# Kernel optimization log

Hardware: AMD Instinct MI355X
Metric: run time of the kernel (lower is better)

Reference implementation:

```python
import jax, jax.numpy as jnp
import numpy as np

N = 50000; F = 128; H = 128; E = 800000; G = 512; C = 1000; CE = 64; L = 128
EPS = 1e-5

def gcn_conv(x, src, dst, W, b, num_nodes):
    # PyG GCNConv: add self loops, sym-normalize, aggregate at dst
    loop = jnp.arange(num_nodes)
    s = jnp.concatenate([src, loop])
    d = jnp.concatenate([dst, loop])
    deg = jax.ops.segment_sum(jnp.ones_like(d, dtype=x.dtype), d, num_segments=num_nodes)
    dinv = jnp.where(deg > 0, jax.lax.rsqrt(deg), 0.0)
    norm = dinv[s] * dinv[d]                      # [E+N]
    h = x @ W                                     # [N,H]
    msg = h[s] * norm[:, None]                    # gather + scale
    return jax.ops.segment_sum(msg, d, num_segments=num_nodes) + b

def layer_norm(x, w, b):
    mu = jnp.mean(x, axis=-1, keepdims=True)
    var = jnp.var(x, axis=-1, keepdims=True)
    return (x - mu) * jax.lax.rsqrt(var + EPS) * w + b

def setup_inputs() -> dict:
    key = jax.random.key(0)
    ks = jax.random.split(key, 16)
    x = jax.random.normal(ks[0], (N, F), dtype=jnp.float32)
    edge_index = jax.random.randint(ks[1], (2, E), 0, N)
    batch = jnp.sort(jax.random.randint(ks[2], (N,), 0, G))
    cell_lines = jax.random.randint(ks[3], (G,), 0, C)
    def kai(k, shape):
        fan_in = shape[0]
        bound = np.sqrt(6.0 / fan_in)
        return jax.random.uniform(k, shape, jnp.float32, -bound, bound)
    return {
        'x': x, 'edge_index': edge_index, 'batch': batch, 'cell_lines': cell_lines,
        'W1': kai(ks[4], (F, H)), 'b1': jnp.zeros((H,), jnp.float32),
        'W2': kai(ks[5], (H, H)), 'b2': jnp.zeros((H,), jnp.float32),
        'emb': jax.random.normal(ks[6], (C, CE), dtype=jnp.float32),
        'Wc': kai(ks[7], (H + CE, H)), 'bc': jnp.zeros((H,), jnp.float32),
        'lnc_w': jnp.ones((H,), jnp.float32), 'lnc_b': jnp.zeros((H,), jnp.float32),
        'Wf1': kai(ks[8], (H, H)), 'bf1': jnp.zeros((H,), jnp.float32),
        'ln1_w': jnp.ones((H,), jnp.float32), 'ln1_b': jnp.zeros((H,), jnp.float32),
        'Wf2': kai(ks[9], (H, L)), 'bf2': jnp.zeros((L,), jnp.float32),
    }

def reference(x, edge_index, batch, cell_lines, W1, b1, W2, b2, emb, Wc, bc,
              lnc_w, lnc_b, Wf1, bf1, ln1_w, ln1_b, Wf2, bf2):
    src, dst = edge_index[0], edge_index[1]
    h = jax.nn.relu(gcn_conv(x, src, dst, W1, b1, N))
    h = jax.nn.relu(gcn_conv(h, src, dst, W2, b2, N))
    g = jax.ops.segment_sum(h, batch, num_segments=G)          # global_add_pool [G,H]
    ce = emb[cell_lines]                                       # [G,CE]
    comb = jnp.concatenate([g, ce], axis=1)
    comb = jax.nn.relu(layer_norm(comb @ Wc + bc, lnc_w, lnc_b))
    out = jax.nn.relu(comb @ Wf1 + bf1)                        # dropout = identity (eval)
    out = layer_norm(out, ln1_w, ln1_b)
    return out @ Wf2 + bf2
```

## Files before the change

### kernel.cpp

```cpp
#include <hip/hip_runtime.h>

#define N_NODES 50000
#define NFEAT 128
#define NEDGE 800000
#define NGRAPH 512
#define NCE 64
#define EPS 1e-5f
#define NBUCK 196
#define EPB 4096
#define BCAP 6144

typedef short s8v __attribute__((ext_vector_type(8)));
typedef float f4v __attribute__((ext_vector_type(4)));

static __device__ __forceinline__ unsigned short f2bf(float f) {
    unsigned int u = __float_as_uint(f);
    unsigned int r = u + 0x7fffu + ((u >> 16) & 1u);
    return (unsigned short)(r >> 16);
}
static __device__ __forceinline__ float bf_lo(unsigned int packed) {
    return __uint_as_float(packed << 16);
}
static __device__ __forceinline__ float bf_hi(unsigned int packed) {
    return __uint_as_float(packed & 0xffff0000u);
}
static __device__ __forceinline__ float bf_us(unsigned short us) {
    return __uint_as_float(((unsigned int)us) << 16);
}

__global__ __launch_bounds__(256) void wcast_kernel(
    const float* __restrict__ W1, const float* __restrict__ W2,
    unsigned short* __restrict__ WT1, unsigned short* __restrict__ WT2,
    int* __restrict__ bucketCursor)
{
    if (blockIdx.x == 0 && blockIdx.y == 0 && threadIdx.x < NBUCK)
        bucketCursor[threadIdx.x] = 0;
    const float* W = blockIdx.y ? W2 : W1;
    unsigned short* WT = blockIdx.y ? WT2 : WT1;
    int idx = blockIdx.x * 256 + threadIdx.x;
    int k = idx >> 7, n = idx & 127;
    WT[n * 128 + k] = f2bf(W[idx]);
}

__global__ __launch_bounds__(256) void bucket_scatter_kernel(
    const int* __restrict__ ei, int* __restrict__ bucketCursor,
    unsigned int* __restrict__ recbuf, int E)
{
    __shared__ int hist[NBUCK];
    __shared__ int lbase[NBUCK];
    __shared__ int gbase[NBUCK];
    __shared__ int cur[NBUCK];
    __shared__ int scanbuf[256];
    __shared__ unsigned int staging[EPB];
    int tid = threadIdx.x;
    if (tid < NBUCK) { hist[tid] = 0; cur[tid] = 0; }
    __syncthreads();

    unsigned int rec[EPB / 256];
    int e0 = blockIdx.x * EPB + tid;
#pragma unroll
    for (int i = 0; i < EPB / 256; ++i) {
        int e = e0 + i * 256;
        if (e < E) {
            unsigned int sv = (unsigned)ei[e];
            unsigned int dv = (unsigned)ei[E + e];
            rec[i] = sv | (dv << 16);
            atomicAdd(&hist[dv >> 8], 1);
        } else {
            rec[i] = 0xffffffffu;
        }
    }
    __syncthreads();
    int v = (tid < NBUCK) ? hist[tid] : 0;
    scanbuf[tid] = v; __syncthreads();
    for (int off = 1; off < 256; off <<= 1) {
        int t = (tid >= off) ? scanbuf[tid - off] : 0;
        __syncthreads();
        scanbuf[tid] += t;
        __syncthreads();
    }
    if (tid < NBUCK) lbase[tid] = scanbuf[tid] - v;
    int total = scanbuf[255];
    if (tid < NBUCK) gbase[tid] = (v > 0) ? atomicAdd(&bucketCursor[tid], v) : 0;
    __syncthreads();
#pragma unroll
    for (int i = 0; i < EPB / 256; ++i) {
        if (rec[i] != 0xffffffffu) {
            int b = rec[i] >> 24;
            int loc = atomicAdd(&cur[b], 1);
            staging[lbase[b] + loc] = rec[i];
        }
    }
    __syncthreads();
    for (int s = tid; s < total; s += 256) {
        unsigned int r = staging[s];
        int b = r >> 24;
        int pos = gbase[b] + (s - lbase[b]);
        if (pos < BCAP) recbuf[(size_t)b * BCAP + pos] = r;
    }
}

__global__ __launch_bounds__(256) void bucket_csr_kernel(
    const unsigned int* __restrict__ recbuf, const int* __restrict__ bucketCursor,
    int* __restrict__ rowbeg, unsigned short* __restrict__ deg,
    float* __restrict__ dinv, unsigned short* __restrict__ colidx)
{
    __shared__ int cnt[256];
    __shared__ int cur[256];
    __shared__ int scanbuf[256];
    __shared__ unsigned short stage[BCAP];
    int b = blockIdx.x, tid = threadIdx.x;
    int base = b * BCAP;
    int len = bucketCursor[b]; if (len > BCAP) len = BCAP;
    cnt[tid] = 0;
    __syncthreads();
    for (int s = tid; s < len; s += 256) {
        unsigned int r = recbuf[base + s];
        atomicAdd(&cnt[(r >> 16) & 255], 1);
    }
    __syncthreads();
    int v = cnt[tid];
    scanbuf[tid] = v; __syncthreads();
    for (int off = 1; off < 256; off <<= 1) {
        int t = (tid >= off) ? scanbuf[tid - off] : 0;
        __syncthreads();
        scanbuf[tid] += t;
        __syncthreads();
    }
    int excl = scanbuf[tid] - v;
    int node = b * 256 + tid;
    if (node < N_NODES) {
        rowbeg[node] = base + excl;
        deg[node] = (unsigned short)v;
        dinv[node] = rsqrtf((float)v + 1.0f);
    }
    cur[tid] = excl;
    __syncthreads();
    for (int s = tid; s < len; s += 256) {
        unsigned int r = recbuf[base + s];
        int pos = atomicAdd(&cur[(r >> 16) & 255], 1);
        stage[pos] = (unsigned short)(r & 0xffffu);
    }
    __syncthreads();
    for (int s = tid; s < len; s += 256) colidx[base + s] = stage[s];
}

template<bool FP32IN>
__global__ __launch_bounds__(256) void gemm_mfma_kernel(
    const void* __restrict__ Ain, const unsigned short* __restrict__ WTg,
    const float* __restrict__ dinv, unsigned short* __restrict__ HS, int nrows)
{
    __shared__ unsigned short as[128 * 128];
    __shared__ unsigned short wt[128 * 128];
    const int tid = threadIdx.x;
    const int row0 = blockIdx.x * 128;

    {
        const uint4* src = reinterpret_cast<const uint4*>(WTg);
        uint4* dst = reinterpret_cast<uint4*>(wt);
#pragma unroll
        for (int i = 0; i < 8; ++i) dst[tid + i * 256] = src[tid + i * 256];
    }
    if (FP32IN) {
        const float* X = (const float*)Ain;
#pragma unroll
        for (int i = 0; i < 16; ++i) {
            int f = tid + i * 256;
            int r = f >> 5, c4 = f & 31;
            int rr = row0 + r; if (rr >= nrows) rr = nrows - 1;
            float4 v = *reinterpret_cast<const float4*>(&X[rr * 128 + c4 * 4]);
            ushort4 o;
            o.x = f2bf(v.x); o.y = f2bf(v.y); o.z = f2bf(v.z); o.w = f2bf(v.w);
            *reinterpret_cast<ushort4*>(&as[r * 128 + c4 * 4]) = o;
        }
    } else {
        const unsigned short* X = (const unsigned short*)Ain;
#pragma unroll
        for (int i = 0; i < 8; ++i) {
            int f = tid + i * 256;
            int r = f >> 4, c8 = f & 15;
            int rr = row0 + r; if (rr >= nrows) rr = nrows - 1;
            *reinterpret_cast<uint4*>(&as[r * 128 + c8 * 8]) =
                *reinterpret_cast<const uint4*>(&X[rr * 128 + c8 * 8]);
        }
    }
    __syncthreads();

    const int w = tid >> 6;
    const int lane = tid & 63;
    const int quad = lane >> 4;
    const int col0 = lane & 15;

    s8v afr[2][4];
#pragma unroll
    for (int rt = 0; rt < 2; ++rt)
#pragma unroll
        for (int kt = 0; kt < 4; ++kt)
            afr[rt][kt] = *reinterpret_cast<const s8v*>(
                &as[(w * 32 + rt * 16 + col0) * 128 + kt * 32 + quad * 8]);

    f4v acc[2][8];
#pragma unroll
    for (int rt = 0; rt < 2; ++rt)
#pragma unroll
        for (int nt = 0; nt < 8; ++nt)
            acc[rt][nt] = (f4v){0.f, 0.f, 0.f, 0.f};

#pragma unroll
    for (int nt = 0; nt < 8; ++nt) {
        s8v bfr[4];
#pragma unroll
        for (int kt = 0; kt < 4; ++kt)
            bfr[kt] = *reinterpret_cast<const s8v*>(
                &wt[(nt * 16 + col0) * 128 + kt * 32 + quad * 8]);
#pragma unroll
        for (int rt = 0; rt < 2; ++rt)
#pragma unroll
            for (int kt = 0; kt < 4; ++kt)
                acc[rt][nt] = __builtin_amdgcn_mfma_f32_16x16x32_bf16(
                    afr[rt][kt], bfr[kt], acc[rt][nt], 0, 0, 0);
    }

    float dv[2][4];
#pragma unroll
    for (int rt = 0; rt < 2; ++rt)
#pragma unroll
        for (int reg = 0; reg < 4; ++reg) {
            int r = row0 + w * 32 + rt * 16 + quad * 4 + reg;
            dv[rt][reg] = (r < nrows) ? dinv[r] : 0.f;
        }

#pragma unroll
    for (int rt = 0; rt < 2; ++rt)
#pragma unroll
        for (int nt = 0; nt < 8; ++nt)
#pragma unroll
            for (int reg = 0; reg < 4; ++reg) {
                int rl = w * 32 + rt * 16 + quad * 4 + reg;
                as[rl * 128 + nt * 16 + col0] = f2bf(acc[rt][nt][reg] * dv[rt][reg]);
            }
    __syncthreads();
#pragma unroll
    for (int i = 0; i < 8; ++i) {
        int f = tid + i * 256;
        int r = f >> 4, c8 = f & 15;
        if (row0 + r < nrows)
            *reinterpret_cast<uint4*>(&HS[(size_t)(row0 + r) * 128 + c8 * 8]) =
                *reinterpret_cast<const uint4*>(&as[r * 128 + c8 * 8]);
    }
}

__global__ __launch_bounds__(256) void aggregate_kernel(
    const uint2* __restrict__ H2,
    const int* __restrict__ rowbeg, const unsigned short* __restrict__ deg,
    const unsigned short* __restrict__ colidx,
    const float* __restrict__ dinv, const float* __restrict__ bias,
    uint2* __restrict__ OUT, int n)
{
    int wid = (blockIdx.x * blockDim.x + threadIdx.x) >> 6;
    int lane = threadIdx.x & 63;
    if (wid >= n) return;
    const int half = lane >> 5;
    const int sub = lane & 31;
    int beg = rowbeg[wid];
    int cnt = (int)deg[wid] + 1;
    float s0 = 0.f, s1 = 0.f, s2 = 0.f, s3 = 0.f;
    float r0 = 0.f, r1 = 0.f, r2 = 0.f, r3 = 0.f;
    for (int base = 0; base < cnt; base += 64) {
        int m = cnt - base; if (m > 64) m = 64;
        int p = base + lane;
        int idx = 0;
        if (lane < m) idx = (p == 0) ? wid : (int)colidx[beg + p - 1];
        int j = 0;
        for (; j + 16 <= m; j += 16) {
            uint2 t[8];
#pragma unroll
            for (int q = 0; q < 8; ++q) {
                int u = __shfl(idx, j + q * 2 + half);
                t[q] = H2[(size_t)u * 32 + sub];
            }
#pragma unroll
            for (int q = 0; q < 8; q += 2) {
                s0 += bf_lo(t[q].x); s1 += bf_hi(t[q].x);
                s2 += bf_lo(t[q].y); s3 += bf_hi(t[q].y);
                r0 += bf_lo(t[q + 1].x); r1 += bf_hi(t[q + 1].x);
                r2 += bf_lo(t[q + 1].y); r3 += bf_hi(t[q + 1].y);
            }
        }
        for (; j + 4 <= m; j += 4) {
            int ua = __shfl(idx, j + half);
            int ub = __shfl(idx, j + 2 + half);
            uint2 ta = H2[(size_t)ua * 32 + sub];
            uint2 tb = H2[(size_t)ub * 32 + sub];
            s0 += bf_lo(ta.x); s1 += bf_hi(ta.x);
            s2 += bf_lo(ta.y); s3 += bf_hi(ta.y);
            r0 += bf_lo(tb.x); r1 += bf_hi(tb.x);
            r2 += bf_lo(tb.y); r3 += bf_hi(tb.y);
        }
        if (j + 2 <= m) {
            int u = __shfl(idx, j + half);
            uint2 t = H2[(size_t)u * 32 + sub];
            s0 += bf_lo(t.x); s1 += bf_hi(t.x);
            s2 += bf_lo(t.y); s3 += bf_hi(t.y);
            j += 2;
        }
        if (j < m) {
            int u = __shfl(idx, j);
            uint2 t; t.x = 0u; t.y = 0u;
            if (half == 0) t = H2[(size_t)u * 32 + sub];
            s0 += bf_lo(t.x); s1 += bf_hi(t.x);
            s2 += bf_lo(t.y); s3 += bf_hi(t.y);
        }
    }
    s0 += r0; s1 += r1; s2 += r2; s3 += r3;
    s0 += __shfl_xor(s0, 32);
    s1 += __shfl_xor(s1, 32);
    s2 += __shfl_xor(s2, 32);
    s3 += __shfl_xor(s3, 32);
    if (half == 0) {
        float sc = dinv[wid];
        float4 bv = *reinterpret_cast<const float4*>(&bias[sub * 4]);
        float o0 = fmaxf(fmaf(s0, sc, bv.x), 0.f);
        float o1 = fmaxf(fmaf(s1, sc, bv.y), 0.f);
        float o2 = fmaxf(fmaf(s2, sc, bv.z), 0.f);
        float o3 = fmaxf(fmaf(s3, sc, bv.w), 0.f);
        uint2 o;
        o.x = (unsigned int)f2bf(o0) | ((unsigned int)f2bf(o1) << 16);
        o.y = (unsigned int)f2bf(o2) | ((unsigned int)f2bf(o3) << 16);
        OUT[(size_t)wid * 32 + sub] = o;
    }
}

__global__ __launch_bounds__(256) void tail_kernel(
    const unsigned short* __restrict__ h2b, const int* __restrict__ batch,
    const int* __restrict__ cell, const float* __restrict__ emb,
    const float* __restrict__ Wc, const float* __restrict__ bc,
    const float* __restrict__ lncw, const float* __restrict__ lncb,
    const float* __restrict__ Wf1, const float* __restrict__ bf1,
    const float* __restrict__ ln1w, const float* __restrict__ ln1b,
    const float* __restrict__ Wf2, const float* __restrict__ bf2,
    float* __restrict__ out)
{
    __shared__ __align__(16) float comb[192];
    __shared__ __align__(16) float part[8][132];
    __shared__ float red[4];
    __shared__ __align__(16) float vec[128];
    const int gi = blockIdx.x;
    const int tid = threadIdx.x;
    const int cg = tid & 31;
    const int ks = tid >> 5;

    int lo = 0, hi = N_NODES;
    while (lo < hi) { int mid = (lo + hi) >> 1; if (batch[mid] < gi) lo = mid + 1; else hi = mid; }
    int lo2 = lo, hi2 = N_NODES;
    while (lo2 < hi2) { int mid = (lo2 + hi2) >> 1; if (batch[mid] < gi + 1) lo2 = mid + 1; else hi2 = mid; }

    {
        int half = tid >> 7;
        int j = tid & 127;
        float acc = 0.f;
        for (int v = lo + half; v < lo2; v += 2)
            acc += bf_us(h2b[(size_t)v * 128 + j]);
        part[half][j] = acc;
    }
    __syncthreads();
    if (tid < 128) comb[tid] = part[0][tid] + part[1][tid];
    else if (tid < 192) comb[tid] = emb[cell[gi] * 64 + (tid - 128)];
    __syncthreads();

    {
        float c[24];
#pragma unroll
        for (int i = 0; i < 6; ++i) {
            float4 t = *reinterpret_cast<const float4*>(&comb[ks * 24 + i * 4]);
            c[i * 4 + 0] = t.x; c[i * 4 + 1] = t.y; c[i * 4 + 2] = t.z; c[i * 4 + 3] = t.w;
        }
        float a0 = 0.f, a1 = 0.f, a2 = 0.f, a3 = 0.f;
#pragma unroll
        for (int i = 0; i < 24; ++i) {
            const float4 w = *reinterpret_cast<const float4*>(&Wc[(ks * 24 + i) * 128 + cg * 4]);
            a0 = fmaf(c[i], w.x, a0);
            a1 = fmaf(c[i], w.y, a1);
            a2 = fmaf(c[i], w.z, a2);
            a3 = fmaf(c[i], w.w, a3);
        }
        float4 o; o.x = a0; o.y = a1; o.z = a2; o.w = a3;
        *reinterpret_cast<float4*>(&part[ks][cg * 4]) = o;
    }
    __syncthreads();
    {
        float y = 0.f;
        if (tid < 128) {
            y = bc[tid];
#pragma unroll
            for (int s = 0; s < 8; ++s) y += part[s][tid];
        }
        float s1 = (tid < 128) ? y : 0.f;
        float s2 = (tid < 128) ? y * y : 0.f;
        if (tid < 128) {
#pragma unroll
            for (int off = 32; off > 0; off >>= 1) {
                s1 += __shfl_down(s1, off);
                s2 += __shfl_down(s2, off);
            }
            if ((tid & 63) == 0) { red[(tid >> 6) * 2] = s1; red[(tid >> 6) * 2 + 1] = s2; }
        }
        __syncthreads();
        float mu = (red[0] + red[2]) * (1.f / 128.f);
        float ms = (red[1] + red[3]) * (1.f / 128.f);
        float var = ms - mu * mu;
        if (tid < 128) {
            float yv = (y - mu) * rsqrtf(var + EPS) * lncw[tid] + lncb[tid];
            vec[tid] = fmaxf(yv, 0.f);
        }
    }
    __syncthreads();

    {
        float c[16];
#pragma unroll
        for (int i = 0; i < 4; ++i) {
            float4 t = *reinterpret_cast<const float4*>(&vec[ks * 16 + i * 4]);
            c[i * 4 + 0] = t.x; c[i * 4 + 1] = t.y; c[i * 4 + 2] = t.z; c[i * 4 + 3] = t.w;
        }
        float a0 = 0.f, a1 = 0.f, a2 = 0.f, a3 = 0.f;
#pragma unroll
        for (int i = 0; i < 16; ++i) {
            const float4 w = *reinterpret_cast<const float4*>(&Wf1[(ks * 16 + i) * 128 + cg * 4]);
            a0 = fmaf(c[i], w.x, a0);
            a1 = fmaf(c[i], w.y, a1);
            a2 = fmaf(c[i], w.z, a2);
            a3 = fmaf(c[i], w.w, a3);
        }
        float4 o; o.x = a0; o.y = a1; o.z = a2; o.w = a3;
        *reinterpret_cast<float4*>(&part[ks][cg * 4]) = o;
    }
    __syncthreads();
    {
        float y = 0.f;
        if (tid < 128) {
            y = bf1[tid];
#pragma unroll
            for (int s = 0; s < 8; ++s) y += part[s][tid];
            y = fmaxf(y, 0.f);
        }
        float s1 = (tid < 128) ? y : 0.f;
        float s2 = (tid < 128) ? y * y : 0.f;
        if (tid < 128) {
#pragma unroll
            for (int off = 32; off > 0; off >>= 1) {
                s1 += __shfl_down(s1, off);
                s2 += __shfl_down(s2, off);
            }
            if ((tid & 63) == 0) { red[(tid >> 6) * 2] = s1; red[(tid >> 6) * 2 + 1] = s2; }
        }
        __syncthreads();
        float mu = (red[0] + red[2]) * (1.f / 128.f);
        float ms = (red[1] + red[3]) * (1.f / 128.f);
        float var = ms - mu * mu;
        if (tid < 128)
            vec[tid] = (y - mu) * rsqrtf(var + EPS) * ln1w[tid] + ln1b[tid];
    }
    __syncthreads();

    {
        float c[16];
#pragma unroll
        for (int i = 0; i < 4; ++i) {
            float4 t = *reinterpret_cast<const float4*>(&vec[ks * 16 + i * 4]);
            c[i * 4 + 0] = t.x; c[i * 4 + 1] = t.y; c[i * 4 + 2] = t.z; c[i * 4 + 3] = t.w;
        }
        float a0 = 0.f, a1 = 0.f, a2 = 0.f, a3 = 0.f;
#pragma unroll
        for (int i = 0; i < 16; ++i) {
            const float4 w = *reinterpret_cast<const float4*>(&Wf2[(ks * 16 + i) * 128 + cg * 4]);
            a0 = fmaf(c[i], w.x, a0);
            a1 = fmaf(c[i], w.y, a1);
            a2 = fmaf(c[i], w.z, a2);
            a3 = fmaf(c[i], w.w, a3);
        }
        float4 o; o.x = a0; o.y = a1; o.z = a2; o.w = a3;
        *reinterpret_cast<float4*>(&part[ks][cg * 4]) = o;
    }
    __syncthreads();
    if (tid < 128) {
        float y = bf2[tid];
#pragma unroll
        for (int s = 0; s < 8; ++s) y += part[s][tid];
        out[gi * 128 + tid] = y;
    }
}

extern "C" void kernel_launch(void* const* d_in, const int* in_sizes, int n_in,
                              void* d_out, int out_size, void* d_ws, size_t ws_size,
                              hipStream_t stream) {
    const float* x    = (const float*)d_in[0];
    const int*   ei   = (const int*)d_in[1];
    const int*   batch= (const int*)d_in[2];
    const int*   cell = (const int*)d_in[3];
    const float* W1   = (const float*)d_in[4];
    const float* b1   = (const float*)d_in[5];
    const float* W2   = (const float*)d_in[6];
    const float* b2   = (const float*)d_in[7];
    const float* emb  = (const float*)d_in[8];
    const float* Wc   = (const float*)d_in[9];
    const float* bc   = (const float*)d_in[10];
    const float* lncw = (const float*)d_in[11];
    const float* lncb = (const float*)d_in[12];
    const float* Wf1  = (const float*)d_in[13];
    const float* bf1  = (const float*)d_in[14];
    const float* ln1w = (const float*)d_in[15];
    const float* ln1b = (const float*)d_in[16];
    const float* Wf2  = (const float*)d_in[17];
    const float* bf2  = (const float*)d_in[18];
    float* out = (float*)d_out;

    char* ws = (char*)d_ws;
    size_t off = 0;
    auto alloc = [&](size_t bytes) { char* p = ws + off; off = (off + bytes + 255) & ~size_t(255); return p; };
    float*          dinv        = (float*)alloc(N_NODES * 4);
    int*            rowbeg      = (int*)  alloc(N_NODES * 4);
    unsigned short* deg         = (unsigned short*)alloc(N_NODES * 2);
    unsigned short* colidx      = (unsigned short*)alloc((size_t)NBUCK * BCAP * 2);
    int*            bucketCursor= (int*)  alloc(NBUCK * 4);
    unsigned int*   recbuf      = (unsigned int*)alloc((size_t)NBUCK * BCAP * 4);
    unsigned short* wt1         = (unsigned short*)alloc(128 * 128 * 2);
    unsigned short* wt2         = (unsigned short*)alloc(128 * 128 * 2);
    unsigned short* hs          = (unsigned short*)alloc((size_t)N_NODES * 128 * 2);
    unsigned short* h1          = (unsigned short*)alloc((size_t)N_NODES * 128 * 2);
    unsigned short* h2b         = (unsigned short*)alloc((size_t)N_NODES * 128 * 2);

    const int nbEdge = (NEDGE + EPB - 1) / EPB;
    const int nbGemm = (N_NODES + 127) / 128;
    const int nbAgg  = (N_NODES + 3) / 4;

    wcast_kernel<<<dim3(64, 2), 256, 0, stream>>>(W1, W2, wt1, wt2, bucketCursor);

    bucket_scatter_kernel<<<nbEdge, 256, 0, stream>>>(ei, bucketCursor, recbuf, NEDGE);
    bucket_csr_kernel<<<NBUCK, 256, 0, stream>>>(recbuf, bucketCursor, rowbeg, deg, dinv, colidx);

    gemm_mfma_kernel<true><<<nbGemm, 256, 0, stream>>>(x, wt1, dinv, hs, N_NODES);
    aggregate_kernel<<<nbAgg, 256, 0, stream>>>((const uint2*)hs, rowbeg, deg, colidx,
                                                dinv, b1, (uint2*)h1, N_NODES);
    gemm_mfma_kernel<false><<<nbGemm, 256, 0, stream>>>(h1, wt2, dinv, hs, N_NODES);
    aggregate_kernel<<<nbAgg, 256, 0, stream>>>((const uint2*)hs, rowbeg, deg, colidx,
                                                dinv, b2, (uint2*)h2b, N_NODES);
    tail_kernel<<<NGRAPH, 256, 0, stream>>>(h2b, batch, cell, emb, Wc, bc, lncw, lncb,
                                            Wf1, bf1, ln1w, ln1b, Wf2, bf2, out);
}
```

Measured before the change: 243.5 us.

## Fuse layer-1 aggregation with layer-2 GEMM in one LDS-resident kernel

```diff
diff --git a/kernel.cpp b/kernel.cpp
--- a/kernel.cpp
+++ b/kernel.cpp
@@ -12,6 +12,7 @@
 
 typedef short s8v __attribute__((ext_vector_type(8)));
 typedef float f4v __attribute__((ext_vector_type(4)));
+typedef float f2v __attribute__((ext_vector_type(2)));
 
 static __device__ __forceinline__ unsigned short f2bf(float f) {
     unsigned int u = __float_as_uint(f);
@@ -26,6 +27,9 @@
 }
 static __device__ __forceinline__ float bf_us(unsigned short us) {
     return __uint_as_float(((unsigned int)us) << 16);
+}
+static __device__ __forceinline__ f2v unpk(unsigned int u) {
+    f2v r; r.x = bf_lo(u); r.y = bf_hi(u); return r;
 }
 
 __global__ __launch_bounds__(256) void wcast_kernel(
@@ -250,6 +254,75 @@
     }
 }
 
+static __device__ __forceinline__ uint2 agg_node(
+    const uint2* __restrict__ H2, const int* __restrict__ rowbeg,
+    const unsigned short* __restrict__ deg, const unsigned short* __restrict__ colidx,
+    const float* __restrict__ dinv, const float* __restrict__ bias,
+    int node, int lane)
+{
+    const int half = lane >> 5;
+    const int sub = lane & 31;
+    const int beg = rowbeg[node];
+    const int cnt = (int)deg[node] + 1;
+    f2v a01 = {0.f, 0.f}, a23 = {0.f, 0.f};
+    f2v b01 = {0.f, 0.f}, b23 = {0.f, 0.f};
+    for (int base = 0; base < cnt; base += 64) {
+        int m = cnt - base; if (m > 64) m = 64;
+        int p = base + lane;
+        int idx = 0;
+        if (lane < m) idx = (p == 0) ? node : (int)colidx[beg + p - 1];
+        int j = 0;
+        for (; j + 16 <= m; j += 16) {
+            uint2 t[8];
+#pragma unroll
+            for (int q = 0; q < 8; ++q) {
+                int u = __shfl(idx, j + q * 2 + half);
+                t[q] = H2[(size_t)u * 32 + sub];
+            }
+#pragma unroll
+            for (int q = 0; q < 8; q += 2) {
+                a01 += unpk(t[q].x);     a23 += unpk(t[q].y);
+                b01 += unpk(t[q + 1].x); b23 += unpk(t[q + 1].y);
+            }
+        }
+        for (; j + 4 <= m; j += 4) {
+            int ua = __shfl(idx, j + half);
+            int ub = __shfl(idx, j + 2 + half);
+            uint2 ta = H2[(size_t)ua * 32 + sub];
+            uint2 tb = H2[(size_t)ub * 32 + sub];
+            a01 += unpk(ta.x); a23 += unpk(ta.y);
+            b01 += unpk(tb.x); b23 += unpk(tb.y);
+        }
+        if (j + 2 <= m) {
+            int u = __shfl(idx, j + half);
+            uint2 t = H2[(size_t)u * 32 + sub];
+            a01 += unpk(t.x); a23 += unpk(t.y);
+            j += 2;
+        }
+        if (j < m) {
+            int u = __shfl(idx, j);
+            uint2 t; t.x = 0u; t.y = 0u;
+            if (half == 0) t = H2[(size_t)u * 32 + sub];
+            a01 += unpk(t.x); a23 += unpk(t.y);
+        }
+    }
+    a01 += b01; a23 += b23;
+    float s0 = a01.x + __shfl_xor(a01.x, 32);
+    float s1 = a01.y + __shfl_xor(a01.y, 32);
+    float s2 = a23.x + __shfl_xor(a23.x, 32);
+    float s3 = a23.y + __shfl_xor(a23.y, 32);
+    float sc = dinv[node];
+    float4 bv = *reinterpret_cast<const float4*>(&bias[sub * 4]);
+    float o0 = fmaxf(fmaf(s0, sc, bv.x), 0.f);
+    float o1 = fmaxf(fmaf(s1, sc, bv.y), 0.f);
+    float o2 = fmaxf(fmaf(s2, sc, bv.z), 0.f);
+    float o3 = fmaxf(fmaf(s3, sc, bv.w), 0.f);
+    uint2 o;
+    o.x = (unsigned int)f2bf(o0) | ((unsigned int)f2bf(o1) << 16);
+    o.y = (unsigned int)f2bf(o2) | ((unsigned int)f2bf(o3) << 16);
+    return o;
+}
+
 __global__ __launch_bounds__(256) void aggregate_kernel(
     const uint2* __restrict__ H2,
     const int* __restrict__ rowbeg, const unsigned short* __restrict__ deg,
@@ -260,74 +333,92 @@
     int wid = (blockIdx.x * blockDim.x + threadIdx.x) >> 6;
     int lane = threadIdx.x & 63;
     if (wid >= n) return;
-    const int half = lane >> 5;
-    const int sub = lane & 31;
-    int beg = rowbeg[wid];
-    int cnt = (int)deg[wid] + 1;
-    float s0 = 0.f, s1 = 0.f, s2 = 0.f, s3 = 0.f;
-    float r0 = 0.f, r1 = 0.f, r2 = 0.f, r3 = 0.f;
-    for (int base = 0; base < cnt; base += 64) {
-        int m = cnt - base; if (m > 64) m = 64;
-        int p = base + lane;
-        int idx = 0;
-        if (lane < m) idx = (p == 0) ? wid : (int)colidx[beg + p - 1];
-        int j = 0;
-        for (; j + 16 <= m; j += 16) {
-            uint2 t[8];
-#pragma unroll
-            for (int q = 0; q < 8; ++q) {
-                int u = __shfl(idx, j + q * 2 + half);
-                t[q] = H2[(size_t)u * 32 + sub];
-            }
-#pragma unroll
-            for (int q = 0; q < 8; q += 2) {
-                s0 += bf_lo(t[q].x); s1 += bf_hi(t[q].x);
-                s2 += bf_lo(t[q].y); s3 += bf_hi(t[q].y);
-                r0 += bf_lo(t[q + 1].x); r1 += bf_hi(t[q + 1].x);
-                r2 += bf_lo(t[q + 1].y); r3 += bf_hi(t[q + 1].y);
-            }
-        }
-        for (; j + 4 <= m; j += 4) {
-            int ua = __shfl(idx, j + half);
-            int ub = __shfl(idx, j + 2 + half);
-            uint2 ta = H2[(size_t)ua * 32 + sub];
-            uint2 tb = H2[(size_t)ub * 32 + sub];
-            s0 += bf_lo(ta.x); s1 += bf_hi(ta.x);
-            s2 += bf_lo(ta.y); s3 += bf_hi(ta.y);
-            r0 += bf_lo(tb.x); r1 += bf_hi(tb.x);
-            r2 += bf_lo(tb.y); r3 += bf_hi(tb.y);
-        }
-        if (j + 2 <= m) {
-            int u = __shfl(idx, j + half);
-            uint2 t = H2[(size_t)u * 32 + sub];
-            s0 += bf_lo(t.x); s1 += bf_hi(t.x);
-            s2 += bf_lo(t.y); s3 += bf_hi(t.y);
-            j += 2;
-        }
-        if (j < m) {
-            int u = __shfl(idx, j);
-            uint2 t; t.x = 0u; t.y = 0u;
-            if (half == 0) t = H2[(size_t)u * 32 + sub];
-            s0 += bf_lo(t.x); s1 += bf_hi(t.x);
-            s2 += bf_lo(t.y); s3 += bf_hi(t.y);
-        }
-    }
-    s0 += r0; s1 += r1; s2 += r2; s3 += r3;
-    s0 += __shfl_xor(s0, 32);
-    s1 += __shfl_xor(s1, 32);
-    s2 += __shfl_xor(s2, 32);
-    s3 += __shfl_xor(s3, 32);
-    if (half == 0) {
-        float sc = dinv[wid];
-        float4 bv = *reinterpret_cast<const float4*>(&bias[sub * 4]);
-        float o0 = fmaxf(fmaf(s0, sc, bv.x), 0.f);
-        float o1 = fmaxf(fmaf(s1, sc, bv.y), 0.f);
-        float o2 = fmaxf(fmaf(s2, sc, bv.z), 0.f);
-        float o3 = fmaxf(fmaf(s3, sc, bv.w), 0.f);
-        uint2 o;
-        o.x = (unsigned int)f2bf(o0) | ((unsigned int)f2bf(o1) << 16);
-        o.y = (unsigned int)f2bf(o2) | ((unsigned int)f2bf(o3) << 16);
-        OUT[(size_t)wid * 32 + sub] = o;
+    uint2 o = agg_node(H2, rowbeg, deg, colidx, dinv, bias, wid, lane);
+    if ((lane >> 5) == 0) OUT[(size_t)wid * 32 + (lane & 31)] = o;
+}
+
+__global__ __launch_bounds__(1024, 8) void fused_agg_gemm_kernel(
+    const uint2* __restrict__ H2, const int* __restrict__ rowbeg,
+    const unsigned short* __restrict__ deg, const unsigned short* __restrict__ colidx,
+    const float* __restrict__ dinv, const float* __restrict__ bias,
+    const unsigned short* __restrict__ WTg, unsigned short* __restrict__ HS2, int n)
+{
+    __shared__ unsigned short as[128 * 128];
+    __shared__ unsigned short wt[128 * 128];
+    const int tid = threadIdx.x;
+    const int row0 = blockIdx.x * 128;
+
+    {
+        const uint4* src = reinterpret_cast<const uint4*>(WTg);
+        uint4* dst = reinterpret_cast<uint4*>(wt);
+        dst[tid] = src[tid];
+        dst[tid + 1024] = src[tid + 1024];
+    }
+
+    const int w16 = tid >> 6;
+    const int lane = tid & 63;
+
+    uint2* asu2 = reinterpret_cast<uint2*>(as);
+#pragma unroll 1
+    for (int i = 0; i < 8; ++i) {
+        int r = w16 * 8 + i;
+        int node = row0 + r;
+        if (node < n) {
+            uint2 o = agg_node(H2, rowbeg, deg, colidx, dinv, bias, node, lane);
+            if ((lane >> 5) == 0) asu2[r * 32 + (lane & 31)] = o;
+        }
+    }
+    __syncthreads();
+
+    const int quad = lane >> 4;
+    const int col0 = lane & 15;
+    const int wr  = w16 >> 1;
+    const int nt0 = (w16 & 1) * 4;
+
+    s8v afr[4];
+#pragma unroll
+    for (int kt = 0; kt < 4; ++kt)
+        afr[kt] = *reinterpret_cast<const s8v*>(
+            &as[(wr * 16 + col0) * 128 + kt * 32 + quad * 8]);
+
+    f4v acc[4];
+#pragma unroll
+    for (int nt = 0; nt < 4; ++nt) acc[nt] = (f4v){0.f, 0.f, 0.f, 0.f};
+
+#pragma unroll
+    for (int nt = 0; nt < 4; ++nt) {
+        s8v bfr[4];
+#pragma unroll
+        for (int kt = 0; kt < 4; ++kt)
+            bfr[kt] = *reinterpret_cast<const s8v*>(
+                &wt[((nt0 + nt) * 16 + col0) * 128 + kt * 32 + quad * 8]);
+#pragma unroll
+        for (int kt = 0; kt < 4; ++kt)
+            acc[nt] = __builtin_amdgcn_mfma_f32_16x16x32_bf16(
+                afr[kt], bfr[kt], acc[nt], 0, 0, 0);
+    }
+
+    float dv[4];
+#pragma unroll
+    for (int reg = 0; reg < 4; ++reg) {
+        int r = row0 + wr * 16 + quad * 4 + reg;
+        dv[reg] = (r < n) ? dinv[r] : 0.f;
+    }
+    __syncthreads();
+#pragma unroll
+    for (int nt = 0; nt < 4; ++nt)
+#pragma unroll
+        for (int reg = 0; reg < 4; ++reg)
+            as[(wr * 16 + quad * 4 + reg) * 128 + (nt0 + nt) * 16 + col0] =
+                f2bf(acc[nt][reg] * dv[reg]);
+    __syncthreads();
+#pragma unroll
+    for (int i = 0; i < 2; ++i) {
+        int f = tid + i * 1024;
+        int r = f >> 4, c8 = f & 15;
+        if (row0 + r < n)
+            *reinterpret_cast<uint4*>(&HS2[(size_t)(row0 + r) * 128 + c8 * 8]) =
+                *reinterpret_cast<const uint4*>(&as[r * 128 + c8 * 8]);
     }
 }
 
@@ -356,15 +447,17 @@
     while (lo2 < hi2) { int mid = (lo2 + hi2) >> 1; if (batch[mid] < gi + 1) lo2 = mid + 1; else hi2 = mid; }
 
     {
-        int half = tid >> 7;
-        int j = tid & 127;
-        float acc = 0.f;
-        for (int v = lo + half; v < lo2; v += 2)
-            acc += bf_us(h2b[(size_t)v * 128 + j]);
-        part[half][j] = acc;
-    }
-    __syncthreads();
-    if (tid < 128) comb[tid] = part[0][tid] + part[1][tid];
+        int q = tid >> 6;
+        int j = tid & 63;
+        const unsigned int* h2u = (const unsigned int*)h2b;
+        f2v acc = {0.f, 0.f};
+        for (int v = lo + q; v < lo2; v += 4)
+            acc += unpk(h2u[(size_t)v * 64 + j]);
+        part[q][j * 2]     = acc.x;
+        part[q][j * 2 + 1] = acc.y;
+    }
+    __syncthreads();
+    if (tid < 128) comb[tid] = (part[0][tid] + part[1][tid]) + (part[2][tid] + part[3][tid]);
     else if (tid < 192) comb[tid] = emb[cell[gi] * 64 + (tid - 128)];
     __syncthreads();
 
@@ -527,7 +620,7 @@
     unsigned short* wt1         = (unsigned short*)alloc(128 * 128 * 2);
     unsigned short* wt2         = (unsigned short*)alloc(128 * 128 * 2);
     unsigned short* hs          = (unsigned short*)alloc((size_t)N_NODES * 128 * 2);
-    unsigned short* h1          = (unsigned short*)alloc((size_t)N_NODES * 128 * 2);
+    unsigned short* hs2         = (unsigned short*)alloc((size_t)N_NODES * 128 * 2);
     unsigned short* h2b         = (unsigned short*)alloc((size_t)N_NODES * 128 * 2);
 
     const int nbEdge = (NEDGE + EPB - 1) / EPB;
@@ -540,10 +633,11 @@
     bucket_csr_kernel<<<NBUCK, 256, 0, stream>>>(recbuf, bucketCursor, rowbeg, deg, dinv, colidx);
 
     gemm_mfma_kernel<true><<<nbGemm, 256, 0, stream>>>(x, wt1, dinv, hs, N_NODES);
-    aggregate_kernel<<<nbAgg, 256, 0, stream>>>((const uint2*)hs, rowbeg, deg, colidx,
-                                                dinv, b1, (uint2*)h1, N_NODES);
-    gemm_mfma_kernel<false><<<nbGemm, 256, 0, stream>>>(h1, wt2, dinv, hs, N_NODES);
-    aggregate_kernel<<<nbAgg, 256, 0, stream>>>((const uint2*)hs, rowbeg, deg, colidx,
+
+    fused_agg_gemm_kernel<<<nbGemm, 1024, 0, stream>>>(
+        (const uint2*)hs, rowbeg, deg, colidx, dinv, b1, wt2, hs2, N_NODES);
+
+    aggregate_kernel<<<nbAgg, 256, 0, stream>>>((const uint2*)hs2, rowbeg, deg, colidx,
                                                 dinv, b2, (uint2*)h2b, N_NODES);
     tail_kernel<<<NGRAPH, 256, 0, stream>>>(h2b, batch, cell, emb, Wc, bc, lncw, lncb,
                                             Wf1, bf1, ln1w, ln1b, Wf2, bf2, out);
```

New measurement: 231.3 us. -5.0%, faster.
